# Kernel tuning notes

Hardware: AMD Instinct MI355X
Metric: run time of the kernel (lower is better)

## Reference

```python
import jax, jax.numpy as jnp
import numpy as np


def _w16_to_4():
    # Constant 4x16 projection from 16 gate logits to {1, A, B, A*B} coefficients
    W = np.zeros((4, 16), np.float32)
    W[0, 8:16] = 1
    W[1, [2, 3, 6, 7]] = 1
    W[1, [8, 9, 12, 13]] = -1
    W[2, [4, 5, 6, 7]] = 1
    W[2, [8, 9, 10, 11]] = -1
    W[3, 1] = 1
    W[3, 6] = -2
    W[3, [2, 4, 7, 14]] = -1
    W[3, [1, 8, 11, 13]] = 1
    W[3, 9] = 2
    return jnp.asarray(W)

W16_TO_4 = _w16_to_4()
G_SPARSITY = 1.0


def _layer(x, idx, w):
    # x: [B, in], idx: [2G] gather indices, w: [16, G]
    B = x.shape[0]
    xg = x[:, idx].reshape(B, -1, 2)          # [B, G, 2]
    A = xg[..., 0]
    Bv = xg[..., 1]
    s = jax.nn.softmax(w * G_SPARSITY, axis=0)  # [16, G]
    w4 = W16_TO_4 @ s                           # [4, G]
    return w4[0] + w4[1] * A + w4[2] * Bv + w4[3] * (A * Bv)  # [B, G]


def setup_inputs() -> dict:
    key = jax.random.key(0)
    B, IN, G, L = 2048, 1024, 16384, 6
    ks = jax.random.split(key, 2 * L + 3)
    inp = {"x": jax.random.uniform(ks[0], (B, IN), dtype=jnp.float32)}
    for l in range(L):
        hi = IN if l == 0 else G
        inp[f"idx{l}"] = jax.random.randint(ks[1 + l], (2 * G,), 0, hi, dtype=jnp.int32)
        inp[f"w{l}"] = jax.random.normal(ks[1 + L + l], (16, G), dtype=jnp.float32)
    inp["lin_w"] = jax.random.normal(ks[-2], (G, 1), dtype=jnp.float32) * 0.01
    inp["lin_b"] = jnp.zeros((1,), dtype=jnp.float32)
    return inp


def reference(x, w0, w1, w2, w3, w4, w5, lin_w, lin_b,
              idx0, idx1, idx2, idx3, idx4, idx5):
    ws = [w0, w1, w2, w3, w4, w5]
    idxs = [idx0, idx1, idx2, idx3, idx4, idx5]
    for w, idx in zip(ws, idxs):
        x = _layer(x, idx, w)
    return x @ lin_w + lin_b  # [B, 1]
```

## Files before the change

kernel.cpp:

```cpp
#include <hip/hip_runtime.h>
#include <hip/hip_fp16.h>

#define G_DIM 16384
#define N_BATCH 2048
#define IN_DIM 1024
#define NLAYER 6
#define THREADS 1024
#define NPAIR 8
#define NCHUNK 4
#define ROWS 4

struct Ptrs {
    const int*   idx[NLAYER];
    const float* w[NLAYER];
};

__device__ __forceinline__ unsigned f2h(float a, float b) {
    __half2 h = __floats2half2_rn(a, b);
    return *reinterpret_cast<unsigned*>(&h);
}

__device__ __forceinline__ float mix_hlh(unsigned a, unsigned b, unsigned c) {
    float d;
    asm("v_fma_mix_f32 %0, %1, %2, %3 op_sel:[1,0,1] op_sel_hi:[1,1,1]"
        : "=v"(d) : "v"(a), "v"(b), "v"(c));
    return d;
}
__device__ __forceinline__ float mix_hhh(unsigned a, unsigned b, unsigned c) {
    float d;
    asm("v_fma_mix_f32 %0, %1, %2, %3 op_sel:[1,1,1] op_sel_hi:[1,1,1]"
        : "=v"(d) : "v"(a), "v"(b), "v"(c));
    return d;
}
__device__ __forceinline__ float mix_lll(unsigned a, unsigned b, unsigned c) {
    float d;
    asm("v_fma_mix_f32 %0, %1, %2, %3 op_sel:[0,0,0] op_sel_hi:[1,1,1]"
        : "=v"(d) : "v"(a), "v"(b), "v"(c));
    return d;
}
__device__ __forceinline__ float mix_lhl(unsigned a, unsigned b, unsigned c) {
    float d;
    asm("v_fma_mix_f32 %0, %1, %2, %3 op_sel:[0,1,0] op_sel_hi:[1,1,1]"
        : "=v"(d) : "v"(a), "v"(b), "v"(c));
    return d;
}
__device__ __forceinline__ float mix_alo(float u, unsigned A, float v) {
    float d;
    asm("v_fma_mix_f32 %0, %1, %2, %3 op_sel:[0,0,0] op_sel_hi:[0,1,0]"
        : "=v"(d) : "v"(u), "v"(A), "v"(v));
    return d;
}
__device__ __forceinline__ float mix_ahi(float u, unsigned A, float v) {
    float d;
    asm("v_fma_mix_f32 %0, %1, %2, %3 op_sel:[0,1,0] op_sel_hi:[0,1,0]"
        : "=v"(d) : "v"(u), "v"(A), "v"(v));
    return d;
}
__device__ __forceinline__ unsigned mix_pack(float u0, float v0, float u1, float v1,
                                             unsigned A) {
    unsigned t;
    asm("v_fma_mixlo_f16 %0, %1, %2, %3 op_sel:[0,0,0] op_sel_hi:[0,1,0]"
        : "=v"(t) : "v"(u0), "v"(A), "v"(v0));
    asm("v_fma_mixhi_f16 %0, %1, %2, %3 op_sel:[0,1,0] op_sel_hi:[0,1,0]"
        : "+v"(t) : "v"(u1), "v"(A), "v"(v1));
    return t;
}

struct PairG { uint2 A0, B0, A1, B1; };

#define GATHER(G, PK)                                     \
    do {                                                  \
        (G).A0 = buf[(PK).x & 0xFFFFu];                   \
        (G).B0 = buf[(PK).x >> 16];                       \
        (G).A1 = buf[(PK).y & 0xFFFFu];                   \
        (G).B1 = buf[(PK).y >> 16];                       \
    } while (0)

__device__ __forceinline__ uint2 gate_fma(uint2 Au, uint2 Bu, unsigned c01, unsigned c23) {
    const float u0 = mix_hlh(c23, Bu.x, c01);
    const float u1 = mix_hhh(c23, Bu.x, c01);
    const float v0 = mix_lll(c23, Bu.x, c01);
    const float v1 = mix_lhl(c23, Bu.x, c01);
    const float u2 = mix_hlh(c23, Bu.y, c01);
    const float u3 = mix_hhh(c23, Bu.y, c01);
    const float v2 = mix_lll(c23, Bu.y, c01);
    const float v3 = mix_lhl(c23, Bu.y, c01);
    const unsigned t01 = mix_pack(u0, v0, u1, v1, Au.x);
    const unsigned t23 = mix_pack(u2, v2, u3, v3, Au.y);
    return make_uint2(t01, t23);
}
__device__ __forceinline__ void gate_acc(uint2 Au, uint2 Bu, unsigned c01, unsigned c23,
                                         float lw, float& a0, float& a1, float& a2, float& a3) {
    const float u0 = mix_hlh(c23, Bu.x, c01);
    const float u1 = mix_hhh(c23, Bu.x, c01);
    const float v0 = mix_lll(c23, Bu.x, c01);
    const float v1 = mix_lhl(c23, Bu.x, c01);
    const float u2 = mix_hlh(c23, Bu.y, c01);
    const float u3 = mix_hhh(c23, Bu.y, c01);
    const float v2 = mix_lll(c23, Bu.y, c01);
    const float v3 = mix_lhl(c23, Bu.y, c01);
    a0 = fmaf(mix_alo(u0, Au.x, v0), lw, a0);
    a1 = fmaf(mix_ahi(u1, Au.x, v1), lw, a1);
    a2 = fmaf(mix_alo(u2, Au.y, v2), lw, a2);
    a3 = fmaf(mix_ahi(u3, Au.y, v3), lw, a3);
}

__device__ __forceinline__ float4 softmax_coef(const float* __restrict__ w, int g) {
    float v[16];
    float m = -1e30f;
#pragma unroll
    for (int k = 0; k < 16; ++k) { v[k] = w[k * G_DIM + g]; m = fmaxf(m, v[k]); }
    float s = 0.f;
#pragma unroll
    for (int k = 0; k < 16; ++k) { v[k] = expf(v[k] - m); s += v[k]; }
    const float inv = 1.f / s;
    float4 c;
    c.x = (v[8]+v[9]+v[10]+v[11]+v[12]+v[13]+v[14]+v[15]) * inv;
    c.y = (v[2]+v[3]+v[6]+v[7] - v[8]-v[9]-v[12]-v[13]) * inv;
    c.z = (v[4]+v[5]+v[6]+v[7] - v[8]-v[9]-v[10]-v[11]) * inv;
    c.w = (v[1]-v[2]-v[4]-2.f*v[6]-v[7]+v[8]+2.f*v[9]+v[11]+v[13]-v[14]) * inv;
    return c;
}

__global__ __launch_bounds__(256) void pack_kernel(Ptrs P, uint2* __restrict__ hcf,
                                                   unsigned* __restrict__ sidx) {
    const int g = blockIdx.x * blockDim.x + threadIdx.x;
    const int l = blockIdx.y;
    const float4 c = softmax_coef(P.w[l], g);
    hcf[(size_t)l * G_DIM + g] = make_uint2(f2h(c.x, c.y), f2h(c.z, c.w));
    const int2 p = ((const int2*)P.idx[l])[g];
    sidx[(size_t)l * G_DIM + g] = (unsigned)p.x | ((unsigned)p.y << 16);
}

__global__ __launch_bounds__(THREADS) void fused_ws_kernel(
    const float* __restrict__ x,
    const uint2* __restrict__ hcf,
    const unsigned* __restrict__ sidx,
    const float* __restrict__ lin_w,
    const float* __restrict__ lin_b,
    float* __restrict__ out)
{
    __shared__ uint4 buf4[G_DIM / 2];
    __shared__ float red[ROWS][THREADS / 64];
    uint2* buf = (uint2*)buf4;

    const int tid  = threadIdx.x;
    const int row0 = blockIdx.x * ROWS;

    for (int i = tid; i < IN_DIM; i += THREADS) {
        const float r0 = x[(size_t)(row0 + 0) * IN_DIM + i];
        const float r1 = x[(size_t)(row0 + 1) * IN_DIM + i];
        const float r2 = x[(size_t)(row0 + 2) * IN_DIM + i];
        const float r3 = x[(size_t)(row0 + 3) * IN_DIM + i];
        buf[i] = make_uint2(f2h(r0, r1), f2h(r2, r3));
    }

    const uint2*  __restrict__ sidx2 = (const uint2*)sidx;
    const uint4*  __restrict__ hcf4  = (const uint4*)hcf;
    const float2* __restrict__ lw2   = (const float2*)lin_w;

    uint2 pkA[2], pkB[2];
    uint4 ccA[2];
#pragma unroll
    for (int j = 0; j < 2; ++j) {
        pkA[j] = sidx2[tid + j * THREADS];
        pkB[j] = sidx2[tid + (2 + j) * THREADS];
        ccA[j] = hcf4 [tid + j * THREADS];
    }

    __syncthreads();

    float a0 = 0.f, a1 = 0.f, a2 = 0.f, a3 = 0.f;

#pragma unroll
    for (int l = 0; l < NLAYER; ++l) {
        uint4 o[NPAIR];
        PairG Gc, Gn;
        GATHER(Gc, pkA[0]);

#pragma unroll
        for (int ch = 0; ch < NCHUNK; ++ch) {
            uint2 pkC[2];
            uint4 ccB[2];
            const bool haveC  = (ch + 2 < NCHUNK) || (l + 1 < NLAYER);
            const bool haveB  = (ch + 1 < NCHUNK) || (l + 1 < NLAYER);
            if (haveC) {
                const int lc = (ch + 2 < NCHUNK) ? l : l + 1;
                const int cc_ = (ch + 2 < NCHUNK) ? ch + 2 : ch + 2 - NCHUNK;
                const uint2* sC = sidx2 + (size_t)lc * (G_DIM / 2);
#pragma unroll
                for (int j = 0; j < 2; ++j) pkC[j] = sC[tid + (cc_ * 2 + j) * THREADS];
            }
            if (haveB) {
                const int lb = (ch + 1 < NCHUNK) ? l : l + 1;
                const int cb = (ch + 1 < NCHUNK) ? ch + 1 : 0;
                const uint4* cB = hcf4 + (size_t)lb * (G_DIM / 2);
#pragma unroll
                for (int j = 0; j < 2; ++j) ccB[j] = cB[tid + (cb * 2 + j) * THREADS];
            }
            float2 lwp[2];
            if (l == NLAYER - 1) {
#pragma unroll
                for (int j = 0; j < 2; ++j) lwp[j] = lw2[tid + (ch * 2 + j) * THREADS];
            }

            GATHER(Gn, pkA[1]);
            if (l < NLAYER - 1) {
                const uint2 g0 = gate_fma(Gc.A0, Gc.B0, ccA[0].x, ccA[0].y);
                const uint2 g1 = gate_fma(Gc.A1, Gc.B1, ccA[0].z, ccA[0].w);
                o[ch * 2] = make_uint4(g0.x, g0.y, g1.x, g1.y);
            } else {
                gate_acc(Gc.A0, Gc.B0, ccA[0].x, ccA[0].y, lwp[0].x, a0, a1, a2, a3);
                gate_acc(Gc.A1, Gc.B1, ccA[0].z, ccA[0].w, lwp[0].y, a0, a1, a2, a3);
            }
            if (ch + 1 < NCHUNK) GATHER(Gc, pkB[0]);
            if (l < NLAYER - 1) {
                const uint2 g0 = gate_fma(Gn.A0, Gn.B0, ccA[1].x, ccA[1].y);
                const uint2 g1 = gate_fma(Gn.A1, Gn.B1, ccA[1].z, ccA[1].w);
                o[ch * 2 + 1] = make_uint4(g0.x, g0.y, g1.x, g1.y);
            } else {
                gate_acc(Gn.A0, Gn.B0, ccA[1].x, ccA[1].y, lwp[1].x, a0, a1, a2, a3);
                gate_acc(Gn.A1, Gn.B1, ccA[1].z, ccA[1].w, lwp[1].y, a0, a1, a2, a3);
            }

#pragma unroll
            for (int j = 0; j < 2; ++j) {
                pkA[j] = pkB[j];
                if (haveC) pkB[j] = pkC[j];
                if (haveB) ccA[j] = ccB[j];
            }
        }

        if (l < NLAYER - 1) {
            __syncthreads();
#pragma unroll
            for (int p = 0; p < NPAIR; ++p) buf4[tid + p * THREADS] = o[p];
            __syncthreads();
        }
    }

#pragma unroll
    for (int off = 32; off > 0; off >>= 1) {
        a0 += __shfl_down(a0, off);
        a1 += __shfl_down(a1, off);
        a2 += __shfl_down(a2, off);
        a3 += __shfl_down(a3, off);
    }
    const int lane = tid & 63, wid = tid >> 6;
    if (lane == 0) { red[0][wid] = a0; red[1][wid] = a1; red[2][wid] = a2; red[3][wid] = a3; }
    __syncthreads();
    if (tid < ROWS) {
        float s = 0.f;
#pragma unroll
        for (int k = 0; k < THREADS / 64; ++k) s += red[tid][k];
        out[row0 + tid] = s + lin_b[0];
    }
}

__global__ __launch_bounds__(THREADS, 1) void fused_fallback_kernel(
    const float* __restrict__ x, Ptrs P,
    const float* __restrict__ lin_w, const float* __restrict__ lin_b,
    float* __restrict__ out)
{
    __shared__ float2 buf[G_DIM];
    __shared__ float red0[THREADS / 64];
    __shared__ float red1[THREADS / 64];
    const int tid  = threadIdx.x;
    const int row0 = blockIdx.x * 2;
    for (int i = tid; i < IN_DIM; i += THREADS)
        buf[i] = make_float2(x[(size_t)row0 * IN_DIM + i],
                             x[(size_t)(row0 + 1) * IN_DIM + i]);
    __syncthreads();
    float2 o[16];
    for (int l = 0; l < NLAYER; ++l) {
        const int2* __restrict__ idxl = (const int2*)P.idx[l];
#pragma unroll
        for (int i = 0; i < 16; ++i) {
            const int g = tid + i * THREADS;
            const int2 p = idxl[g];
            const float4 c = softmax_coef(P.w[l], g);
            const float2 Ap = buf[p.x];
            const float2 Bp = buf[p.y];
            o[i].x = fmaf(fmaf(c.w, Bp.x, c.y), Ap.x, fmaf(c.z, Bp.x, c.x));
            o[i].y = fmaf(fmaf(c.w, Bp.y, c.y), Ap.y, fmaf(c.z, Bp.y, c.x));
        }
        __syncthreads();
#pragma unroll
        for (int i = 0; i < 16; ++i) buf[tid + i * THREADS] = o[i];
        __syncthreads();
    }
    float a0 = 0.f, a1 = 0.f;
#pragma unroll
    for (int i = 0; i < 16; ++i) {
        const int g = tid + i * THREADS;
        const float lw = lin_w[g];
        const float2 bv = buf[g];
        a0 = fmaf(bv.x, lw, a0);
        a1 = fmaf(bv.y, lw, a1);
    }
#pragma unroll
    for (int off = 32; off > 0; off >>= 1) {
        a0 += __shfl_down(a0, off);
        a1 += __shfl_down(a1, off);
    }
    const int lane = tid & 63, wid = tid >> 6;
    if (lane == 0) { red0[wid] = a0; red1[wid] = a1; }
    __syncthreads();
    if (tid == 0) {
        float s0 = 0.f, s1 = 0.f;
#pragma unroll
        for (int k = 0; k < THREADS / 64; ++k) { s0 += red0[k]; s1 += red1[k]; }
        const float lb = lin_b[0];
        out[row0]     = s0 + lb;
        out[row0 + 1] = s1 + lb;
    }
}

extern "C" void kernel_launch(void* const* d_in, const int* in_sizes, int n_in,
                              void* d_out, int out_size, void* d_ws, size_t ws_size,
                              hipStream_t stream) {
    const float* x = (const float*)d_in[0];
    Ptrs P;
    for (int l = 0; l < NLAYER; ++l) {
        P.idx[l] = (const int*)d_in[1 + 2 * l];
        P.w[l]   = (const float*)d_in[2 + 2 * l];
    }
    const float* lin_w = (const float*)d_in[13];
    const float* lin_b = (const float*)d_in[14];
    float* out = (float*)d_out;

    const size_t hcf_bytes  = (size_t)NLAYER * G_DIM * sizeof(uint2);
    const size_t sidx_bytes = (size_t)NLAYER * G_DIM * sizeof(unsigned);
    if (ws_size >= hcf_bytes + sidx_bytes) {
        uint2*    hcf  = (uint2*)d_ws;
        unsigned* sidx = (unsigned*)((char*)d_ws + hcf_bytes);
        dim3 cgrid(G_DIM / 256, NLAYER);
        pack_kernel<<<cgrid, 256, 0, stream>>>(P, hcf, sidx);
        fused_ws_kernel<<<N_BATCH / ROWS, THREADS, 0, stream>>>(
            x, hcf, sidx, lin_w, lin_b, out);
    } else {
        fused_fallback_kernel<<<N_BATCH / 2, THREADS, 0, stream>>>(
            x, P, lin_w, lin_b, out);
    }
}
```

Before: 52.91 us.

## Process two row groups per block with cross-group prefetch of indices and coefficients

Each block now handles two groups of four batch rows in sequence rather than one, halving the grid to 256 blocks. The index and coefficient prefetch pipeline carries over from the last layer of the first group into layer 0 of the second, and the second group's input rows are loaded up front and staged into shared memory during the first group's reduction. The aim is to cut block launch and pipeline ramp-up costs and to reuse prefetch state. In exchange, 256 blocks of 1024 threads may underfill a 256-CU device, and per-block work is serialized.

```diff
diff --git a/kernel.cpp b/kernel.cpp
--- a/kernel.cpp
+++ b/kernel.cpp
@@ -9,6 +9,7 @@
 #define NPAIR 8
 #define NCHUNK 4
 #define ROWS 4
+#define NGRP 2
 
 struct Ptrs {
     const int*   idx[NLAYER];
@@ -144,15 +145,18 @@
     __shared__ float red[ROWS][THREADS / 64];
     uint2* buf = (uint2*)buf4;
 
-    const int tid  = threadIdx.x;
-    const int row0 = blockIdx.x * ROWS;
-
-    for (int i = tid; i < IN_DIM; i += THREADS) {
-        const float r0 = x[(size_t)(row0 + 0) * IN_DIM + i];
-        const float r1 = x[(size_t)(row0 + 1) * IN_DIM + i];
-        const float r2 = x[(size_t)(row0 + 2) * IN_DIM + i];
-        const float r3 = x[(size_t)(row0 + 3) * IN_DIM + i];
-        buf[i] = make_uint2(f2h(r0, r1), f2h(r2, r3));
+    const int tid   = threadIdx.x;
+    const int rbase = blockIdx.x * (NGRP * ROWS);
+
+    float x1[ROWS];
+    {
+        float x0[ROWS];
+#pragma unroll
+        for (int r = 0; r < ROWS; ++r) {
+            x0[r] = x[(size_t)(rbase + r) * IN_DIM + tid];
+            x1[r] = x[(size_t)(rbase + ROWS + r) * IN_DIM + tid];
+        }
+        buf[tid] = make_uint2(f2h(x0[0], x0[1]), f2h(x0[2], x0[3]));
     }
 
     const uint2*  __restrict__ sidx2 = (const uint2*)sidx;
@@ -170,90 +174,99 @@
 
     __syncthreads();
 
-    float a0 = 0.f, a1 = 0.f, a2 = 0.f, a3 = 0.f;
-
-#pragma unroll
-    for (int l = 0; l < NLAYER; ++l) {
-        uint4 o[NPAIR];
-        PairG Gc, Gn;
-        GATHER(Gc, pkA[0]);
-
-#pragma unroll
-        for (int ch = 0; ch < NCHUNK; ++ch) {
-            uint2 pkC[2];
-            uint4 ccB[2];
-            const bool haveC  = (ch + 2 < NCHUNK) || (l + 1 < NLAYER);
-            const bool haveB  = (ch + 1 < NCHUNK) || (l + 1 < NLAYER);
-            if (haveC) {
-                const int lc = (ch + 2 < NCHUNK) ? l : l + 1;
-                const int cc_ = (ch + 2 < NCHUNK) ? ch + 2 : ch + 2 - NCHUNK;
-                const uint2* sC = sidx2 + (size_t)lc * (G_DIM / 2);
-#pragma unroll
-                for (int j = 0; j < 2; ++j) pkC[j] = sC[tid + (cc_ * 2 + j) * THREADS];
+#pragma unroll
+    for (int grp = 0; grp < NGRP; ++grp) {
+        float a0 = 0.f, a1 = 0.f, a2 = 0.f, a3 = 0.f;
+
+#pragma unroll
+        for (int l = 0; l < NLAYER; ++l) {
+            const int  lnext = (l + 1 == NLAYER) ? 0 : l + 1;
+            const bool more  = (l + 1 < NLAYER) || (grp + 1 < NGRP);
+            uint4 o[NPAIR];
+            PairG Gc, Gn;
+            GATHER(Gc, pkA[0]);
+
+#pragma unroll
+            for (int ch = 0; ch < NCHUNK; ++ch) {
+                uint2 pkC[2];
+                uint4 ccB[2];
+                const bool haveC = (ch + 2 < NCHUNK) || more;
+                const bool haveB = (ch + 1 < NCHUNK) || more;
+                if (haveC) {
+                    const int lc  = (ch + 2 < NCHUNK) ? l : lnext;
+                    const int cc_ = (ch + 2 < NCHUNK) ? ch + 2 : ch + 2 - NCHUNK;
+                    const uint2* sC = sidx2 + (size_t)lc * (G_DIM / 2);
+#pragma unroll
+                    for (int j = 0; j < 2; ++j) pkC[j] = sC[tid + (cc_ * 2 + j) * THREADS];
+                }
+                if (haveB) {
+                    const int lb = (ch + 1 < NCHUNK) ? l : lnext;
+                    const int cb = (ch + 1 < NCHUNK) ? ch + 1 : 0;
+                    const uint4* cB = hcf4 + (size_t)lb * (G_DIM / 2);
+#pragma unroll
+                    for (int j = 0; j < 2; ++j) ccB[j] = cB[tid + (cb * 2 + j) * THREADS];
+                }
+                float2 lwp[2];
+                if (l == NLAYER - 1) {
+#pragma unroll
+                    for (int j = 0; j < 2; ++j) lwp[j] = lw2[tid + (ch * 2 + j) * THREADS];
+                }
+
+                GATHER(Gn, pkA[1]);
+                if (l < NLAYER - 1) {
+                    const uint2 g0 = gate_fma(Gc.A0, Gc.B0, ccA[0].x, ccA[0].y);
+                    const uint2 g1 = gate_fma(Gc.A1, Gc.B1, ccA[0].z, ccA[0].w);
+                    o[ch * 2] = make_uint4(g0.x, g0.y, g1.x, g1.y);
+                } else {
+                    gate_acc(Gc.A0, Gc.B0, ccA[0].x, ccA[0].y, lwp[0].x, a0, a1, a2, a3);
+                    gate_acc(Gc.A1, Gc.B1, ccA[0].z, ccA[0].w, lwp[0].y, a0, a1, a2, a3);
+                }
+                if (ch + 1 < NCHUNK) GATHER(Gc, pkB[0]);
+                if (l < NLAYER - 1) {
+                    const uint2 g0 = gate_fma(Gn.A0, Gn.B0, ccA[1].x, ccA[1].y);
+                    const uint2 g1 = gate_fma(Gn.A1, Gn.B1, ccA[1].z, ccA[1].w);
+                    o[ch * 2 + 1] = make_uint4(g0.x, g0.y, g1.x, g1.y);
+                } else {
+                    gate_acc(Gn.A0, Gn.B0, ccA[1].x, ccA[1].y, lwp[1].x, a0, a1, a2, a3);
+                    gate_acc(Gn.A1, Gn.B1, ccA[1].z, ccA[1].w, lwp[1].y, a0, a1, a2, a3);
+                }
+
+#pragma unroll
+                for (int j = 0; j < 2; ++j) {
+                    if (ch + 1 < NCHUNK || more) pkA[j] = pkB[j];
+                    if (haveC) pkB[j] = pkC[j];
+                    if (haveB) ccA[j] = ccB[j];
+                }
             }
-            if (haveB) {
-                const int lb = (ch + 1 < NCHUNK) ? l : l + 1;
-                const int cb = (ch + 1 < NCHUNK) ? ch + 1 : 0;
-                const uint4* cB = hcf4 + (size_t)lb * (G_DIM / 2);
-#pragma unroll
-                for (int j = 0; j < 2; ++j) ccB[j] = cB[tid + (cb * 2 + j) * THREADS];
+
+            if (l < NLAYER - 1) {
+                __syncthreads();
+#pragma unroll
+                for (int p = 0; p < NPAIR; ++p) buf4[tid + p * THREADS] = o[p];
+                __syncthreads();
             }
-            float2 lwp[2];
-            if (l == NLAYER - 1) {
-#pragma unroll
-                for (int j = 0; j < 2; ++j) lwp[j] = lw2[tid + (ch * 2 + j) * THREADS];
-            }
-
-            GATHER(Gn, pkA[1]);
-            if (l < NLAYER - 1) {
-                const uint2 g0 = gate_fma(Gc.A0, Gc.B0, ccA[0].x, ccA[0].y);
-                const uint2 g1 = gate_fma(Gc.A1, Gc.B1, ccA[0].z, ccA[0].w);
-                o[ch * 2] = make_uint4(g0.x, g0.y, g1.x, g1.y);
-            } else {
-                gate_acc(Gc.A0, Gc.B0, ccA[0].x, ccA[0].y, lwp[0].x, a0, a1, a2, a3);
-                gate_acc(Gc.A1, Gc.B1, ccA[0].z, ccA[0].w, lwp[0].y, a0, a1, a2, a3);
-            }
-            if (ch + 1 < NCHUNK) GATHER(Gc, pkB[0]);
-            if (l < NLAYER - 1) {
-                const uint2 g0 = gate_fma(Gn.A0, Gn.B0, ccA[1].x, ccA[1].y);
-                const uint2 g1 = gate_fma(Gn.A1, Gn.B1, ccA[1].z, ccA[1].w);
-                o[ch * 2 + 1] = make_uint4(g0.x, g0.y, g1.x, g1.y);
-            } else {
-                gate_acc(Gn.A0, Gn.B0, ccA[1].x, ccA[1].y, lwp[1].x, a0, a1, a2, a3);
-                gate_acc(Gn.A1, Gn.B1, ccA[1].z, ccA[1].w, lwp[1].y, a0, a1, a2, a3);
-            }
-
-#pragma unroll
-            for (int j = 0; j < 2; ++j) {
-                pkA[j] = pkB[j];
-                if (haveC) pkB[j] = pkC[j];
-                if (haveB) ccA[j] = ccB[j];
-            }
-        }
-
-        if (l < NLAYER - 1) {
-            __syncthreads();
-#pragma unroll
-            for (int p = 0; p < NPAIR; ++p) buf4[tid + p * THREADS] = o[p];
-            __syncthreads();
-        }
-    }
-
-#pragma unroll
-    for (int off = 32; off > 0; off >>= 1) {
-        a0 += __shfl_down(a0, off);
-        a1 += __shfl_down(a1, off);
-        a2 += __shfl_down(a2, off);
-        a3 += __shfl_down(a3, off);
-    }
-    const int lane = tid & 63, wid = tid >> 6;
-    if (lane == 0) { red[0][wid] = a0; red[1][wid] = a1; red[2][wid] = a2; red[3][wid] = a3; }
-    __syncthreads();
-    if (tid < ROWS) {
-        float s = 0.f;
-#pragma unroll
-        for (int k = 0; k < THREADS / 64; ++k) s += red[tid][k];
-        out[row0 + tid] = s + lin_b[0];
+        }
+
+#pragma unroll
+        for (int off = 32; off > 0; off >>= 1) {
+            a0 += __shfl_down(a0, off);
+            a1 += __shfl_down(a1, off);
+            a2 += __shfl_down(a2, off);
+            a3 += __shfl_down(a3, off);
+        }
+        const int lane = tid & 63, wid = tid >> 6;
+        __syncthreads();
+        if (lane == 0) { red[0][wid] = a0; red[1][wid] = a1; red[2][wid] = a2; red[3][wid] = a3; }
+        if (grp + 1 < NGRP) {
+            buf[tid] = make_uint2(f2h(x1[0], x1[1]), f2h(x1[2], x1[3]));
+        }
+        __syncthreads();
+        if (tid < ROWS) {
+            float s = 0.f;
+#pragma unroll
+            for (int k = 0; k < THREADS / 64; ++k) s += red[tid][k];
+            out[rbase + grp * ROWS + tid] = s + lin_b[0];
+        }
     }
 }
 
@@ -336,7 +349,7 @@
         unsigned* sidx = (unsigned*)((char*)d_ws + hcf_bytes);
         dim3 cgrid(G_DIM / 256, NLAYER);
         pack_kernel<<<cgrid, 256, 0, stream>>>(P, hcf, sidx);
-        fused_ws_kernel<<<N_BATCH / ROWS, THREADS, 0, stream>>>(
+        fused_ws_kernel<<<N_BATCH / (NGRP * ROWS), THREADS, 0, stream>>>(
             x, hcf, sidx, lin_w, lin_b, out);
     } else {
         fused_fallback_kernel<<<N_BATCH / 2, THREADS, 0, stream>>>(
```

Result: slower. 83.87 us (+58.5%).
